# Performance work log

Hardware: AMD Instinct MI355X
Metric: run time of the kernel (lower is better)

The kernel has to match this reference:

```python
import jax, jax.numpy as jnp
import numpy as np
from jax import lax

INPUT_SIZE = 3
HIDDEN = 32
SEQ = 24
BATCH = 131072
FC1 = 16


def setup_inputs() -> dict:
    key = jax.random.key(0)
    ks = jax.random.split(key, 9)
    s_ih = 1.0 / np.sqrt(HIDDEN)
    # PyTorch LSTM params: weight_ih (4H, input), weight_hh (4H, H), biases (4H,)
    return {
        "x": jax.random.normal(ks[0], (BATCH, SEQ, INPUT_SIZE), dtype=jnp.float32),
        "w_ih": jax.random.uniform(ks[1], (4 * HIDDEN, INPUT_SIZE), minval=-s_ih, maxval=s_ih, dtype=jnp.float32),
        "w_hh": jax.random.uniform(ks[2], (4 * HIDDEN, HIDDEN), minval=-s_ih, maxval=s_ih, dtype=jnp.float32),
        "b_ih": jax.random.uniform(ks[3], (4 * HIDDEN,), minval=-s_ih, maxval=s_ih, dtype=jnp.float32),
        "b_hh": jax.random.uniform(ks[4], (4 * HIDDEN,), minval=-s_ih, maxval=s_ih, dtype=jnp.float32),
        "w1": jax.random.uniform(ks[5], (FC1, HIDDEN), minval=-s_ih, maxval=s_ih, dtype=jnp.float32),
        "b1": jax.random.uniform(ks[6], (FC1,), minval=-s_ih, maxval=s_ih, dtype=jnp.float32),
        "w2": jax.random.uniform(ks[7], (1, FC1), minval=-0.25, maxval=0.25, dtype=jnp.float32),
        "b2": jax.random.uniform(ks[8], (1,), minval=-0.25, maxval=0.25, dtype=jnp.float32),
    }


def reference(x, w_ih, w_hh, b_ih, b_hh, w1, b1, w2, b2):
    B = x.shape[0]
    b = b_ih + b_hh  # fuse the two bias vectors

    def step(carry, xt):
        h, c = carry
        # gates: (B, 4H) in PyTorch order [i, f, g, o]
        gates = xt @ w_ih.T + h @ w_hh.T + b
        i, f, g, o = jnp.split(gates, 4, axis=-1)
        c_new = jax.nn.sigmoid(f) * c + jax.nn.sigmoid(i) * jnp.tanh(g)
        h_new = jax.nn.sigmoid(o) * jnp.tanh(c_new)
        return (h_new, c_new), None

    h0 = jnp.zeros((B, HIDDEN), dtype=x.dtype)
    c0 = jnp.zeros((B, HIDDEN), dtype=x.dtype)
    xs = jnp.transpose(x, (1, 0, 2))  # (T, B, F)
    (h_last, _), _ = lax.scan(step, (h0, c0), xs)

    # Head: Linear(H,16) -> ReLU -> Dropout(identity in eval) -> Linear(16,1)
    hid = jax.nn.relu(h_last @ w1.T + b1)
    logit = hid @ w2.T + b2  # (B, 1)
    return logit
```

## Files before the change

kernel.cpp:

```cpp
#include <hip/hip_runtime.h>


typedef _Float16 f16x8 __attribute__((ext_vector_type(8)));
typedef _Float16 f16x4 __attribute__((ext_vector_type(4)));
typedef _Float16 f16x2 __attribute__((ext_vector_type(2)));
typedef float f32x4 __attribute__((ext_vector_type(4)));
typedef float f32x2 __attribute__((ext_vector_type(2)));

#define L2E 1.4426950408889634f

#if __has_builtin(__builtin_amdgcn_mfma_f32_16x16x16f16)
#define HAVE_MFMA16 1
#else
#define HAVE_MFMA16 0
#endif

__device__ __forceinline__ float fexp2(float v) { return __builtin_amdgcn_exp2f(v); }
__device__ __forceinline__ float frcp(float v)  { return __builtin_amdgcn_rcpf(v); }

__global__ __launch_bounds__(256, 4)
void lstm_fused(const float* __restrict__ x,
                const float* __restrict__ w_ih,
                const float* __restrict__ w_hh,
                const float* __restrict__ b_ih,
                const float* __restrict__ b_hh,
                const float* __restrict__ w1,
                const float* __restrict__ b1,
                const float* __restrict__ w2,
                const float* __restrict__ b2,
                float* __restrict__ out)
{
    __shared__ int2  xq[24 * 128];
    __shared__ float w1s[512];
    __shared__ float b1s[16];
    __shared__ float w2s[16];
    __shared__ float b2s;

    const int tid  = threadIdx.x;
    const int lane = tid & 63;
    const int wv   = tid >> 6;
    const int c    = lane & 15;
    const int g    = lane >> 4;
    const int blockBase = blockIdx.x * 128;

    for (int i = tid; i < 512; i += 256) w1s[i] = w1[i];
    if (tid < 16) { b1s[tid] = b1[tid]; w2s[tid] = w2[tid]; }
    if (tid == 16) b2s = b2[0];

    for (int it = 0; it < 12; ++it) {
        int p = tid + it * 256;
        int n = p / 24;
        int t = p - n * 24;
        const float* xp = x + ((blockBase + n) * 24 + t) * 3;
        union { f16x4 h; int2 i2; } tq;
        tq.h[0] = (_Float16)xp[0];
        tq.h[1] = (_Float16)xp[1];
        tq.h[2] = (_Float16)xp[2];
        tq.h[3] = (_Float16)1.0f;
        xq[t * 128 + n] = tq.i2;
    }

    f16x8 whh[8];
#if HAVE_MFMA16
    f16x4 wib[8];
#else
    f16x8 wib[8];
#endif
    const int ubase = 8 * (c >> 2) + (c & 3);
#pragma unroll
    for (int G = 0; G < 4; ++G) {
        const float scale = (G == 2) ? (2.f * L2E) : L2E;
#pragma unroll
        for (int p = 0; p < 2; ++p) {
            const int row = G * 32 + ubase + 4 * p;
            const float* wr = w_hh + row * 32 + g * 8;
            f16x8 a;
#pragma unroll
            for (int e = 0; e < 8; ++e) a[e] = (_Float16)(wr[e] * scale);
            whh[G * 2 + p] = a;
            _Float16 c0 = 0, c1 = 0, c2 = 0, c3 = 0;
            if (g == 0) {
                c0 = (_Float16)(w_ih[row * 3 + 0] * scale);
                c1 = (_Float16)(w_ih[row * 3 + 1] * scale);
                c2 = (_Float16)(w_ih[row * 3 + 2] * scale);
                c3 = (_Float16)((b_ih[row] + b_hh[row]) * scale);
            }
#if HAVE_MFMA16
            f16x4 bb = {c0, c1, c2, c3};
#else
            f16x8 bb = {c0, c1, c2, c3, 0, 0, 0, 0};
#endif
            wib[G * 2 + p] = bb;
        }
    }

    __syncthreads();

    f32x2 cz = {0.f, 0.f};
    f32x2 cst2[8];
#pragma unroll
    for (int q = 0; q < 8; ++q) cst2[q] = cz;
    union hu_t { f16x2 p2[4]; f16x8 v; int4 i4; } hreg[2];
    hreg[0].i4 = make_int4(0, 0, 0, 0);
    hreg[1].i4 = make_int4(0, 0, 0, 0);

    const int n0 = wv * 16 + c;
    int2 xv[2];
    xv[0] = xq[n0];
    xv[1] = xq[n0 + 64];

#pragma unroll 1
    for (int t = 0; t < 24; ++t) {
        const int tn = (t < 23) ? t + 1 : 23;
        int2 xn0 = xq[tn * 128 + n0];
        int2 xn1 = xq[tn * 128 + n0 + 64];

#pragma unroll
        for (int s = 0; s < 2; ++s) {
            f32x4 acc[2][4];
            const f32x4 z = {0.f, 0.f, 0.f, 0.f};
            f16x8 hf = hreg[s].v;
#pragma unroll
            for (int p = 0; p < 2; ++p)
#pragma unroll
                for (int G = 0; G < 4; ++G)
                    acc[p][G] = __builtin_amdgcn_mfma_f32_16x16x32_f16(
                        whh[2 * G + p], hf, z, 0, 0, 0);
            {
                int xlo = (g == 0) ? xv[s].x : 0;
                int xhi = (g == 0) ? xv[s].y : 0;
#if HAVE_MFMA16
                union { int2 i2; f16x4 v; } xu;
                xu.i2 = make_int2(xlo, xhi);
                f16x4 xf = xu.v;
#else
                union { int4 i4; f16x8 v; } xu;
                xu.i4 = make_int4(xlo, xhi, 0, 0);
                f16x8 xf = xu.v;
#endif
#pragma unroll
                for (int p = 0; p < 2; ++p)
#pragma unroll
                    for (int G = 0; G < 4; ++G)
#if HAVE_MFMA16
                        acc[p][G] = __builtin_amdgcn_mfma_f32_16x16x16f16(
                            wib[2 * G + p], xf, acc[p][G], 0, 0, 0);
#else
                        acc[p][G] = __builtin_amdgcn_mfma_f32_16x16x32_f16(
                            wib[2 * G + p], xf, acc[p][G], 0, 0, 0);
#endif
            }

            f32x2 ew[4];
#pragma unroll
            for (int q = 0; q < 4; ++q) {
                const int p = q >> 1, j = q & 1;
                ew[q][0] = fexp2(-acc[p][3][2 * j]);
                ew[q][1] = fexp2(-acc[p][3][2 * j + 1]);
            }
            f32x2 ex[4], ey[4], ef[4];
#pragma unroll
            for (int q = 0; q < 4; ++q) {
                const int p = q >> 1, j = q & 1;
                ex[q][0] = fexp2(-acc[p][0][2 * j]); ex[q][1] = fexp2(-acc[p][0][2 * j + 1]);
                ey[q][0] = fexp2( acc[p][2][2 * j]); ey[q][1] = fexp2( acc[p][2][2 * j + 1]);
                ef[q][0] = fexp2(-acc[p][1][2 * j]); ef[q][1] = fexp2(-acc[p][1][2 * j + 1]);
            }
            const f32x2 one = {1.f, 1.f};
            const f32x2 K2  = {2.f * L2E, 2.f * L2E};
            f32x2 axy[4], efp[4], r1[4];
#pragma unroll
            for (int q = 0; q < 4; ++q) {
                axy[q] = (one + ex[q]) * (one + ey[q]);
                efp[q] = one + ef[q];
                f32x2 dd = axy[q] * efp[q];
                r1[q][0] = frcp(dd[0]); r1[q][1] = frcp(dd[1]);
            }
            f32x2 ez[4];
#pragma unroll
            for (int q = 0; q < 4; ++q) {
                f32x2 igs = (ey[q] * K2 - K2) * efp[q] * r1[q];
                f32x2 fs  = axy[q] * r1[q];
                cst2[s * 4 + q] = fs * cst2[s * 4 + q] + igs;
                ez[q][0] = fexp2(cst2[s * 4 + q][0]);
                ez[q][1] = fexp2(cst2[s * 4 + q][1]);
            }
#pragma unroll
            for (int q = 0; q < 4; ++q) {
                f32x2 d2 = (one + ew[q]) * (one + ez[q]);
                f32x2 r2; r2[0] = frcp(d2[0]); r2[1] = frcp(d2[1]);
                f32x2 hn = (ez[q] - one) * r2;
                f16x2 hh; hh[0] = (_Float16)hn[0]; hh[1] = (_Float16)hn[1];
                hreg[s].p2[q] = hh;
            }
        }
        xv[0] = xn0;
        xv[1] = xn1;
    }

#pragma unroll
    for (int s = 0; s < 2; ++s) {
        float hfin[8];
#pragma unroll
        for (int d = 0; d < 8; ++d) hfin[d] = (float)hreg[s].v[d];
        float hid[16];
#pragma unroll
        for (int q = 0; q < 16; ++q) {
            const float4* wrow = (const float4*)(w1s + q * 32 + g * 8);
            float4 wa = wrow[0], wb = wrow[1];
            float sm = wa.x * hfin[0] + wa.y * hfin[1] + wa.z * hfin[2] + wa.w * hfin[3]
                     + wb.x * hfin[4] + wb.y * hfin[5] + wb.z * hfin[6] + wb.w * hfin[7];
            sm += __shfl_xor(sm, 16);
            sm += __shfl_xor(sm, 32);
            hid[q] = sm;
        }
        float po = b2s;
#pragma unroll
        for (int q = 0; q < 16; ++q)
            po = fmaf(fmaxf(hid[q] + b1s[q], 0.f), w2s[q], po);
        if (g == 0) out[blockBase + s * 64 + n0] = po;
    }
}

extern "C" void kernel_launch(void* const* d_in, const int* in_sizes, int n_in,
                              void* d_out, int out_size, void* d_ws, size_t ws_size,
                              hipStream_t stream) {
    (void)in_sizes; (void)n_in; (void)d_ws; (void)ws_size; (void)out_size;
    const float* x    = (const float*)d_in[0];
    const float* w_ih = (const float*)d_in[1];
    const float* w_hh = (const float*)d_in[2];
    const float* b_ih = (const float*)d_in[3];
    const float* b_hh = (const float*)d_in[4];
    const float* w1   = (const float*)d_in[5];
    const float* b1   = (const float*)d_in[6];
    const float* w2   = (const float*)d_in[7];
    const float* b2   = (const float*)d_in[8];
    float* outp = (float*)d_out;

    dim3 grid(131072 / 128);
    dim3 block(256);
    hipLaunchKernelGGL(lstm_fused, grid, block, 0, stream,
                       x, w_ih, w_hh, b_ih, b_hh, w1, b1, w2, b2, outp);
}
```

Measured before the change: 101.1 us.

## Software-pipeline MFMA of one sub-batch with activations of the other

Restructures the time loop so the MFMA gate computation for sub-batch B is issued while sub-batch A's activations run, and A's next-step MFMAs are issued right after its activations, with a peeled prologue and epilogue. The aim is to hide MFMA latency behind transcendental VALU work. Keeping two accumulator sets live raises register pressure, so launch bounds drop from 4 to 3 waves per SIMD, which may reduce occupancy.

New measurement: 95.55 us. 1.06x faster.

```diff
diff --git a/kernel.cpp b/kernel.cpp
--- a/kernel.cpp
+++ b/kernel.cpp
@@ -18,7 +18,7 @@
 __device__ __forceinline__ float fexp2(float v) { return __builtin_amdgcn_exp2f(v); }
 __device__ __forceinline__ float frcp(float v)  { return __builtin_amdgcn_rcpf(v); }
 
-__global__ __launch_bounds__(256, 4)
+__global__ __launch_bounds__(256, 3)
 void lstm_fused(const float* __restrict__ x,
                 const float* __restrict__ w_ih,
                 const float* __restrict__ w_hh,
@@ -109,94 +109,102 @@
     xv[0] = xq[n0];
     xv[1] = xq[n0 + 64];
 
+    auto MFMA_STEP = [&](const f16x8& hf, const int2& xvs, f32x4 (&acc)[2][4]) {
+        const f32x4 z = {0.f, 0.f, 0.f, 0.f};
+#pragma unroll
+        for (int p = 0; p < 2; ++p)
+#pragma unroll
+            for (int G = 0; G < 4; ++G)
+                acc[p][G] = __builtin_amdgcn_mfma_f32_16x16x32_f16(
+                    whh[2 * G + p], hf, z, 0, 0, 0);
+        int xlo = (g == 0) ? xvs.x : 0;
+        int xhi = (g == 0) ? xvs.y : 0;
+#if HAVE_MFMA16
+        union { int2 i2; f16x4 v; } xu;
+        xu.i2 = make_int2(xlo, xhi);
+        f16x4 xf = xu.v;
+#else
+        union { int4 i4; f16x8 v; } xu;
+        xu.i4 = make_int4(xlo, xhi, 0, 0);
+        f16x8 xf = xu.v;
+#endif
+#pragma unroll
+        for (int p = 0; p < 2; ++p)
+#pragma unroll
+            for (int G = 0; G < 4; ++G)
+#if HAVE_MFMA16
+                acc[p][G] = __builtin_amdgcn_mfma_f32_16x16x16f16(
+                    wib[2 * G + p], xf, acc[p][G], 0, 0, 0);
+#else
+                acc[p][G] = __builtin_amdgcn_mfma_f32_16x16x32_f16(
+                    wib[2 * G + p], xf, acc[p][G], 0, 0, 0);
+#endif
+    };
+
+    auto ACT_STEP = [&](f32x4 (&acc)[2][4], int sb, hu_t& hr) {
+        f32x2 ew[4];
+#pragma unroll
+        for (int q = 0; q < 4; ++q) {
+            const int p = q >> 1, j = q & 1;
+            ew[q][0] = fexp2(-acc[p][3][2 * j]);
+            ew[q][1] = fexp2(-acc[p][3][2 * j + 1]);
+        }
+        f32x2 ex[4], ey[4], ef[4];
+#pragma unroll
+        for (int q = 0; q < 4; ++q) {
+            const int p = q >> 1, j = q & 1;
+            ex[q][0] = fexp2(-acc[p][0][2 * j]); ex[q][1] = fexp2(-acc[p][0][2 * j + 1]);
+            ey[q][0] = fexp2( acc[p][2][2 * j]); ey[q][1] = fexp2( acc[p][2][2 * j + 1]);
+            ef[q][0] = fexp2(-acc[p][1][2 * j]); ef[q][1] = fexp2(-acc[p][1][2 * j + 1]);
+        }
+        const f32x2 one = {1.f, 1.f};
+        const f32x2 K2  = {2.f * L2E, 2.f * L2E};
+        f32x2 axy[4], efp[4], r1[4];
+#pragma unroll
+        for (int q = 0; q < 4; ++q) {
+            axy[q] = (one + ex[q]) * (one + ey[q]);
+            efp[q] = one + ef[q];
+            f32x2 dd = axy[q] * efp[q];
+            r1[q][0] = frcp(dd[0]); r1[q][1] = frcp(dd[1]);
+        }
+        f32x2 ez[4];
+#pragma unroll
+        for (int q = 0; q < 4; ++q) {
+            f32x2 igs = (ey[q] * K2 - K2) * efp[q] * r1[q];
+            f32x2 fs  = axy[q] * r1[q];
+            cst2[sb + q] = fs * cst2[sb + q] + igs;
+            ez[q][0] = fexp2(cst2[sb + q][0]);
+            ez[q][1] = fexp2(cst2[sb + q][1]);
+        }
+#pragma unroll
+        for (int q = 0; q < 4; ++q) {
+            f32x2 d2 = (one + ew[q]) * (one + ez[q]);
+            f32x2 r2; r2[0] = frcp(d2[0]); r2[1] = frcp(d2[1]);
+            f32x2 hn = (ez[q] - one) * r2;
+            f16x2 hh; hh[0] = (_Float16)hn[0]; hh[1] = (_Float16)hn[1];
+            hr.p2[q] = hh;
+        }
+    };
+
+    f32x4 accA[2][4], accB[2][4];
+
+    MFMA_STEP(hreg[0].v, xv[0], accA);
+
 #pragma unroll 1
-    for (int t = 0; t < 24; ++t) {
-        const int tn = (t < 23) ? t + 1 : 23;
-        int2 xn0 = xq[tn * 128 + n0];
-        int2 xn1 = xq[tn * 128 + n0 + 64];
-
-#pragma unroll
-        for (int s = 0; s < 2; ++s) {
-            f32x4 acc[2][4];
-            const f32x4 z = {0.f, 0.f, 0.f, 0.f};
-            f16x8 hf = hreg[s].v;
-#pragma unroll
-            for (int p = 0; p < 2; ++p)
-#pragma unroll
-                for (int G = 0; G < 4; ++G)
-                    acc[p][G] = __builtin_amdgcn_mfma_f32_16x16x32_f16(
-                        whh[2 * G + p], hf, z, 0, 0, 0);
-            {
-                int xlo = (g == 0) ? xv[s].x : 0;
-                int xhi = (g == 0) ? xv[s].y : 0;
-#if HAVE_MFMA16
-                union { int2 i2; f16x4 v; } xu;
-                xu.i2 = make_int2(xlo, xhi);
-                f16x4 xf = xu.v;
-#else
-                union { int4 i4; f16x8 v; } xu;
-                xu.i4 = make_int4(xlo, xhi, 0, 0);
-                f16x8 xf = xu.v;
-#endif
-#pragma unroll
-                for (int p = 0; p < 2; ++p)
-#pragma unroll
-                    for (int G = 0; G < 4; ++G)
-#if HAVE_MFMA16
-                        acc[p][G] = __builtin_amdgcn_mfma_f32_16x16x16f16(
-                            wib[2 * G + p], xf, acc[p][G], 0, 0, 0);
-#else
-                        acc[p][G] = __builtin_amdgcn_mfma_f32_16x16x32_f16(
-                            wib[2 * G + p], xf, acc[p][G], 0, 0, 0);
-#endif
-            }
-
-            f32x2 ew[4];
-#pragma unroll
-            for (int q = 0; q < 4; ++q) {
-                const int p = q >> 1, j = q & 1;
-                ew[q][0] = fexp2(-acc[p][3][2 * j]);
-                ew[q][1] = fexp2(-acc[p][3][2 * j + 1]);
-            }
-            f32x2 ex[4], ey[4], ef[4];
-#pragma unroll
-            for (int q = 0; q < 4; ++q) {
-                const int p = q >> 1, j = q & 1;
-                ex[q][0] = fexp2(-acc[p][0][2 * j]); ex[q][1] = fexp2(-acc[p][0][2 * j + 1]);
-                ey[q][0] = fexp2( acc[p][2][2 * j]); ey[q][1] = fexp2( acc[p][2][2 * j + 1]);
-                ef[q][0] = fexp2(-acc[p][1][2 * j]); ef[q][1] = fexp2(-acc[p][1][2 * j + 1]);
-            }
-            const f32x2 one = {1.f, 1.f};
-            const f32x2 K2  = {2.f * L2E, 2.f * L2E};
-            f32x2 axy[4], efp[4], r1[4];
-#pragma unroll
-            for (int q = 0; q < 4; ++q) {
-                axy[q] = (one + ex[q]) * (one + ey[q]);
-                efp[q] = one + ef[q];
-                f32x2 dd = axy[q] * efp[q];
-                r1[q][0] = frcp(dd[0]); r1[q][1] = frcp(dd[1]);
-            }
-            f32x2 ez[4];
-#pragma unroll
-            for (int q = 0; q < 4; ++q) {
-                f32x2 igs = (ey[q] * K2 - K2) * efp[q] * r1[q];
-                f32x2 fs  = axy[q] * r1[q];
-                cst2[s * 4 + q] = fs * cst2[s * 4 + q] + igs;
-                ez[q][0] = fexp2(cst2[s * 4 + q][0]);
-                ez[q][1] = fexp2(cst2[s * 4 + q][1]);
-            }
-#pragma unroll
-            for (int q = 0; q < 4; ++q) {
-                f32x2 d2 = (one + ew[q]) * (one + ez[q]);
-                f32x2 r2; r2[0] = frcp(d2[0]); r2[1] = frcp(d2[1]);
-                f32x2 hn = (ez[q] - one) * r2;
-                f16x2 hh; hh[0] = (_Float16)hn[0]; hh[1] = (_Float16)hn[1];
-                hreg[s].p2[q] = hh;
-            }
-        }
+    for (int t = 0; t < 23; ++t) {
+        int2 xn0 = xq[(t + 1) * 128 + n0];
+        int2 xn1 = xq[(t + 1) * 128 + n0 + 64];
+
+        MFMA_STEP(hreg[1].v, xv[1], accB);
+        ACT_STEP(accA, 0, hreg[0]);
+        ACT_STEP(accB, 4, hreg[1]);
         xv[0] = xn0;
         xv[1] = xn1;
-    }
+        MFMA_STEP(hreg[0].v, xv[0], accA);
+    }
+    MFMA_STEP(hreg[1].v, xv[1], accB);
+    ACT_STEP(accA, 0, hreg[0]);
+    ACT_STEP(accB, 4, hreg[1]);
 
 #pragma unroll
     for (int s = 0; s < 2; ++s) {
```

## Stage recurrent weights in LDS and restructure step schedule with sched barriers

Applied to the files above, without the earlier changes.

Moves the fp16 recurrent weight fragments from per-thread registers into shared memory, written once by the first wave and reloaded from LDS every timestep. Both sub-batches' recurrent MFMAs now share each weight load, and sched_barriers impose a fixed order on the gate nonlinearity phases. The head weights are read from global memory instead of LDS. The aim is to cut VGPR pressure and interleave independent work, at the cost of extra LDS traffic inside the recurrent loop.

New measurement: 96.59 us. 1.05x faster.

```diff
diff --git a/kernel.cpp b/kernel.cpp
--- a/kernel.cpp
+++ b/kernel.cpp
@@ -8,6 +8,7 @@
 typedef float f32x2 __attribute__((ext_vector_type(2)));
 
 #define L2E 1.4426950408889634f
+#define SBAR() __builtin_amdgcn_sched_barrier(0)
 
 #if __has_builtin(__builtin_amdgcn_mfma_f32_16x16x16f16)
 #define HAVE_MFMA16 1
@@ -30,11 +31,8 @@
                 const float* __restrict__ b2,
                 float* __restrict__ out)
 {
-    __shared__ int2  xq[24 * 128];
-    __shared__ float w1s[512];
-    __shared__ float b1s[16];
-    __shared__ float w2s[16];
-    __shared__ float b2s;
+    __shared__ int2 xq[24 * 128];
+    __shared__ int4 whhs[8 * 64];
 
     const int tid  = threadIdx.x;
     const int lane = tid & 63;
@@ -42,10 +40,6 @@
     const int c    = lane & 15;
     const int g    = lane >> 4;
     const int blockBase = blockIdx.x * 128;
-
-    for (int i = tid; i < 512; i += 256) w1s[i] = w1[i];
-    if (tid < 16) { b1s[tid] = b1[tid]; w2s[tid] = w2[tid]; }
-    if (tid == 16) b2s = b2[0];
 
     for (int it = 0; it < 12; ++it) {
         int p = tid + it * 256;
@@ -60,24 +54,34 @@
         xq[t * 128 + n] = tq.i2;
     }
 
-    f16x8 whh[8];
+    const int ubase = 8 * (c >> 2) + (c & 3);
+    if (tid < 64) {
+#pragma unroll
+        for (int G = 0; G < 4; ++G) {
+            const float scale = (G == 2) ? (2.f * L2E) : L2E;
+#pragma unroll
+            for (int p = 0; p < 2; ++p) {
+                const int row = G * 32 + ubase + 4 * p;
+                const float* wr = w_hh + row * 32 + g * 8;
+                union { f16x8 h; int4 i4; } a;
+#pragma unroll
+                for (int e = 0; e < 8; ++e) a.h[e] = (_Float16)(wr[e] * scale);
+                whhs[(G * 2 + p) * 64 + c * 4 + g] = a.i4;
+            }
+        }
+    }
+
 #if HAVE_MFMA16
     f16x4 wib[8];
 #else
     f16x8 wib[8];
 #endif
-    const int ubase = 8 * (c >> 2) + (c & 3);
 #pragma unroll
     for (int G = 0; G < 4; ++G) {
         const float scale = (G == 2) ? (2.f * L2E) : L2E;
 #pragma unroll
         for (int p = 0; p < 2; ++p) {
             const int row = G * 32 + ubase + 4 * p;
-            const float* wr = w_hh + row * 32 + g * 8;
-            f16x8 a;
-#pragma unroll
-            for (int e = 0; e < 8; ++e) a[e] = (_Float16)(wr[e] * scale);
-            whh[G * 2 + p] = a;
             _Float16 c0 = 0, c1 = 0, c2 = 0, c3 = 0;
             if (g == 0) {
                 c0 = (_Float16)(w_ih[row * 3 + 0] * scale);
@@ -108,6 +112,7 @@
     int2 xv[2];
     xv[0] = xq[n0];
     xv[1] = xq[n0 + 64];
+    unsigned woff = (unsigned)(c * 4 + g);
 
 #pragma unroll 1
     for (int t = 0; t < 24; ++t) {
@@ -115,59 +120,63 @@
         int2 xn0 = xq[tn * 128 + n0];
         int2 xn1 = xq[tn * 128 + n0 + 64];
 
+        asm volatile("" : "+v"(woff));
+
+        f32x4 acc[2][2][4];
+        const f32x4 z = {0.f, 0.f, 0.f, 0.f};
+        f16x8 hfA = hreg[0].v;
+        f16x8 hfB = hreg[1].v;
+#pragma unroll
+        for (int G = 0; G < 4; ++G)
+#pragma unroll
+            for (int p = 0; p < 2; ++p) {
+                union { int4 i4; f16x8 h; } fr;
+                fr.i4 = whhs[(2 * G + p) * 64 + woff];
+                acc[0][p][G] = __builtin_amdgcn_mfma_f32_16x16x32_f16(
+                    fr.h, hfA, z, 0, 0, 0);
+                acc[1][p][G] = __builtin_amdgcn_mfma_f32_16x16x32_f16(
+                    fr.h, hfB, z, 0, 0, 0);
+            }
 #pragma unroll
         for (int s = 0; s < 2; ++s) {
-            f32x4 acc[2][4];
-            const f32x4 z = {0.f, 0.f, 0.f, 0.f};
-            f16x8 hf = hreg[s].v;
-#pragma unroll
-            for (int p = 0; p < 2; ++p)
-#pragma unroll
-                for (int G = 0; G < 4; ++G)
-                    acc[p][G] = __builtin_amdgcn_mfma_f32_16x16x32_f16(
-                        whh[2 * G + p], hf, z, 0, 0, 0);
-            {
-                int xlo = (g == 0) ? xv[s].x : 0;
-                int xhi = (g == 0) ? xv[s].y : 0;
-#if HAVE_MFMA16
-                union { int2 i2; f16x4 v; } xu;
-                xu.i2 = make_int2(xlo, xhi);
-                f16x4 xf = xu.v;
-#else
-                union { int4 i4; f16x8 v; } xu;
-                xu.i4 = make_int4(xlo, xhi, 0, 0);
-                f16x8 xf = xu.v;
-#endif
+            int xlo = (g == 0) ? xv[s].x : 0;
+            int xhi = (g == 0) ? xv[s].y : 0;
+#if HAVE_MFMA16
+            union { int2 i2; f16x4 v; } xu;
+            xu.i2 = make_int2(xlo, xhi);
+            f16x4 xf = xu.v;
+#else
+            union { int4 i4; f16x8 v; } xu;
+            xu.i4 = make_int4(xlo, xhi, 0, 0);
+            f16x8 xf = xu.v;
+#endif
+#pragma unroll
+            for (int G = 0; G < 4; ++G)
 #pragma unroll
                 for (int p = 0; p < 2; ++p)
-#pragma unroll
-                    for (int G = 0; G < 4; ++G)
-#if HAVE_MFMA16
-                        acc[p][G] = __builtin_amdgcn_mfma_f32_16x16x16f16(
-                            wib[2 * G + p], xf, acc[p][G], 0, 0, 0);
-#else
-                        acc[p][G] = __builtin_amdgcn_mfma_f32_16x16x32_f16(
-                            wib[2 * G + p], xf, acc[p][G], 0, 0, 0);
-#endif
-            }
-
-            f32x2 ew[4];
+#if HAVE_MFMA16
+                    acc[s][p][G] = __builtin_amdgcn_mfma_f32_16x16x16f16(
+                        wib[2 * G + p], xf, acc[s][p][G], 0, 0, 0);
+#else
+                    acc[s][p][G] = __builtin_amdgcn_mfma_f32_16x16x32_f16(
+                        wib[2 * G + p], xf, acc[s][p][G], 0, 0, 0);
+#endif
+        }
+        SBAR();
+
+        const f32x2 one = {1.f, 1.f};
+        const f32x2 K2  = {2.f * L2E, 2.f * L2E};
+#pragma unroll
+        for (int s = 0; s < 2; ++s) {
+            f32x2 ex[4], ey[4], ef[4];
 #pragma unroll
             for (int q = 0; q < 4; ++q) {
                 const int p = q >> 1, j = q & 1;
-                ew[q][0] = fexp2(-acc[p][3][2 * j]);
-                ew[q][1] = fexp2(-acc[p][3][2 * j + 1]);
-            }
-            f32x2 ex[4], ey[4], ef[4];
-#pragma unroll
-            for (int q = 0; q < 4; ++q) {
-                const int p = q >> 1, j = q & 1;
-                ex[q][0] = fexp2(-acc[p][0][2 * j]); ex[q][1] = fexp2(-acc[p][0][2 * j + 1]);
-                ey[q][0] = fexp2( acc[p][2][2 * j]); ey[q][1] = fexp2( acc[p][2][2 * j + 1]);
-                ef[q][0] = fexp2(-acc[p][1][2 * j]); ef[q][1] = fexp2(-acc[p][1][2 * j + 1]);
-            }
-            const f32x2 one = {1.f, 1.f};
-            const f32x2 K2  = {2.f * L2E, 2.f * L2E};
+                ex[q][0] = fexp2(-acc[s][p][0][2 * j]); ex[q][1] = fexp2(-acc[s][p][0][2 * j + 1]);
+                ey[q][0] = fexp2( acc[s][p][2][2 * j]); ey[q][1] = fexp2( acc[s][p][2][2 * j + 1]);
+                ef[q][0] = fexp2(-acc[s][p][1][2 * j]); ef[q][1] = fexp2(-acc[s][p][1][2 * j + 1]);
+            }
+            SBAR();
             f32x2 axy[4], efp[4], r1[4];
 #pragma unroll
             for (int q = 0; q < 4; ++q) {
@@ -176,6 +185,15 @@
                 f32x2 dd = axy[q] * efp[q];
                 r1[q][0] = frcp(dd[0]); r1[q][1] = frcp(dd[1]);
             }
+            SBAR();
+            f32x2 ew[4];
+#pragma unroll
+            for (int q = 0; q < 4; ++q) {
+                const int p = q >> 1, j = q & 1;
+                ew[q][0] = fexp2(-acc[s][p][3][2 * j]);
+                ew[q][1] = fexp2(-acc[s][p][3][2 * j + 1]);
+            }
+            SBAR();
             f32x2 ez[4];
 #pragma unroll
             for (int q = 0; q < 4; ++q) {
@@ -185,6 +203,7 @@
                 ez[q][0] = fexp2(cst2[s * 4 + q][0]);
                 ez[q][1] = fexp2(cst2[s * 4 + q][1]);
             }
+            SBAR();
 #pragma unroll
             for (int q = 0; q < 4; ++q) {
                 f32x2 d2 = (one + ew[q]) * (one + ez[q]);
@@ -193,6 +212,7 @@
                 f16x2 hh; hh[0] = (_Float16)hn[0]; hh[1] = (_Float16)hn[1];
                 hreg[s].p2[q] = hh;
             }
+            SBAR();
         }
         xv[0] = xn0;
         xv[1] = xn1;
@@ -206,7 +226,7 @@
         float hid[16];
 #pragma unroll
         for (int q = 0; q < 16; ++q) {
-            const float4* wrow = (const float4*)(w1s + q * 32 + g * 8);
+            const float4* wrow = (const float4*)(w1 + q * 32 + g * 8);
             float4 wa = wrow[0], wb = wrow[1];
             float sm = wa.x * hfin[0] + wa.y * hfin[1] + wa.z * hfin[2] + wa.w * hfin[3]
                      + wb.x * hfin[4] + wb.y * hfin[5] + wb.z * hfin[6] + wb.w * hfin[7];
@@ -214,10 +234,10 @@
             sm += __shfl_xor(sm, 32);
             hid[q] = sm;
         }
-        float po = b2s;
+        float po = b2[0];
 #pragma unroll
         for (int q = 0; q < 16; ++q)
-            po = fmaf(fmaxf(hid[q] + b1s[q], 0.f), w2s[q], po);
+            po = fmaf(fmaxf(hid[q] + b1[q], 0.f), w2[q], po);
         if (g == 0) out[blockBase + s * 64 + n0] = po;
     }
 }
```
